# Optimization experiments

Hardware: AMD Instinct MI355X
Metric: run time of the kernel (lower is better)

## Reference

```python
import jax, jax.numpy as jnp
import numpy as np


def setup_inputs() -> dict:
    key = jax.random.key(0)
    k1, k2 = jax.random.split(key)
    query_features = jax.random.normal(k1, (8, 2048, 256), dtype=jnp.float32)   # (B, S, D)
    support_weights = jax.random.normal(k2, (20, 256), dtype=jnp.float32)       # (N, D)
    return {"query_features": query_features, "support_weights": support_weights}


def reference(query_features, support_weights):
    # Original: transpose query to (B, D, S), repeat channels n_cls times,
    # grouped conv1d with groups = n_cls*D, group_size=1, kernel_size=1, padding=0.
    # That is exactly a per-(class, channel) scale of the query features.
    B, S, D = query_features.shape
    N = support_weights.shape[0]
    q = jnp.transpose(query_features, (0, 2, 1))            # (B, D, S)
    # out[b, n, c, s] = q[b, c, s] * w[n, c]
    out = q[:, None, :, :] * support_weights[None, :, :, None]  # (B, N, D, S)
    return out.reshape(B * N, D, S)                          # (B*N, D, S)
```

## Files before the change

### kernel.cpp

```cpp
#include <hip/hip_runtime.h>


namespace {
constexpr int kB = 8;
constexpr int kS = 2048;
constexpr int kD = 256;
constexpr int kN = 20;
constexpr int TS = 512;
constexpr int TC = 16;
constexpr int NSPLIT = 2;
constexpr int NPB = kN / NSPLIT;
constexpr int PTS = TS + 4;

typedef float v4f __attribute__((ext_vector_type(4)));
}

__global__ __launch_bounds__(256)
void frw_kernel(const float* __restrict__ q, const float* __restrict__ w,
                float* __restrict__ out) {
  const int s0 = blockIdx.x * TS;
  const int c0 = blockIdx.y * TC;
  const int b  = blockIdx.z >> 1;
  const int n0 = (blockIdx.z & 1) * NPB;
  const int t  = threadIdx.x;

  __shared__ float tile[TC][PTS];
  __shared__ float ws[NPB][TC];

  for (int i = t; i < NPB * TC; i += 256) {
    const int n  = i / TC;
    const int cc = i % TC;
    ws[n][cc] = w[(n0 + n) * kD + c0 + cc];
  }

  {
    const int lane4 = t & 3;
    const int srow  = t >> 2;
    const int cvec  = lane4 * 4;
#pragma unroll
    for (int k = 0; k < 8; ++k) {
      const int ss = srow + k * 64;
      const float4 v = *reinterpret_cast<const float4*>(
          &q[((size_t)b * kS + (size_t)(s0 + ss)) * kD + (c0 + cvec)]);
      tile[cvec + 0][ss] = v.x;
      tile[cvec + 1][ss] = v.y;
      tile[cvec + 2][ss] = v.z;
      tile[cvec + 3][ss] = v.w;
    }
  }
  __syncthreads();

  const int half = t >> 7;
  const int soff = (t & 127) * 4;
  for (int nn = 0; nn < NPB; ++nn) {
    const int n = n0 + nn;
    const size_t base_bn = ((size_t)(b * kN + n)) * kD;
#pragma unroll
    for (int rg = 0; rg < TC / 2; ++rg) {
      const int r = rg * 2 + half;
      const float sc = ws[nn][r];
      const float4 v = *reinterpret_cast<const float4*>(&tile[r][soff]);
      v4f o;
      o.x = v.x * sc;
      o.y = v.y * sc;
      o.z = v.z * sc;
      o.w = v.w * sc;
      __builtin_nontemporal_store(o, reinterpret_cast<v4f*>(
          &out[(base_bn + (size_t)(c0 + r)) * kS + (size_t)(s0 + soff)]));
    }
  }
}

extern "C" void kernel_launch(void* const* d_in, const int* in_sizes, int n_in,
                              void* d_out, int out_size, void* d_ws, size_t ws_size,
                              hipStream_t stream) {
  const float* q = (const float*)d_in[0];
  const float* w = (const float*)d_in[1];
  float* out = (float*)d_out;

  dim3 grid(kS / TS, kD / TC, kB * NSPLIT);
  frw_kernel<<<grid, 256, 0, stream>>>(q, w, out);
}
```

Before: 342.8 us.

## Tile over full sequence with 8 channels and per-wave contiguous row writes

Each block now loads all 2048 sequence positions for 8 channels into shared memory, instead of 512 positions for 16 channels. Each wave then writes whole 8KB output rows for 20 (class, channel) pairs. The aim is longer contiguous store streams and fewer blocks re-reading scale weights. In exchange it uses more shared memory per block (about 66KB), launches half as many blocks, and reads the input as narrower 32-byte segments.

Measured after the change: 348.9 us. Within noise of the previous version (+1.8%).

```diff
diff --git a/kernel.cpp b/kernel.cpp
--- a/kernel.cpp
+++ b/kernel.cpp
@@ -6,11 +6,10 @@
 constexpr int kS = 2048;
 constexpr int kD = 256;
 constexpr int kN = 20;
-constexpr int TS = 512;
-constexpr int TC = 16;
+constexpr int TC = 8;
 constexpr int NSPLIT = 2;
 constexpr int NPB = kN / NSPLIT;
-constexpr int PTS = TS + 4;
+constexpr int PTS = kS + 4;
 
 typedef float v4f __attribute__((ext_vector_type(4)));
 }
@@ -18,30 +17,27 @@
 __global__ __launch_bounds__(256)
 void frw_kernel(const float* __restrict__ q, const float* __restrict__ w,
                 float* __restrict__ out) {
-  const int s0 = blockIdx.x * TS;
-  const int c0 = blockIdx.y * TC;
-  const int b  = blockIdx.z >> 1;
-  const int n0 = (blockIdx.z & 1) * NPB;
+  const int c0 = blockIdx.x * TC;
+  const int b  = blockIdx.y >> 1;
+  const int n0 = (blockIdx.y & 1) * NPB;
   const int t  = threadIdx.x;
 
   __shared__ float tile[TC][PTS];
   __shared__ float ws[NPB][TC];
 
-  for (int i = t; i < NPB * TC; i += 256) {
-    const int n  = i / TC;
-    const int cc = i % TC;
-    ws[n][cc] = w[(n0 + n) * kD + c0 + cc];
+  if (t < NPB * TC) {
+    ws[t / TC][t % TC] = w[(n0 + t / TC) * kD + c0 + (t % TC)];
   }
 
   {
-    const int lane4 = t & 3;
-    const int srow  = t >> 2;
-    const int cvec  = lane4 * 4;
+    const int lane2 = t & 1;
+    const int srow  = t >> 1;
+    const int cvec  = lane2 * 4;
 #pragma unroll
-    for (int k = 0; k < 8; ++k) {
-      const int ss = srow + k * 64;
+    for (int k = 0; k < 16; ++k) {
+      const int ss = srow + k * 128;
       const float4 v = *reinterpret_cast<const float4*>(
-          &q[((size_t)b * kS + (size_t)(s0 + ss)) * kD + (c0 + cvec)]);
+          &q[((size_t)b * kS + (size_t)ss) * kD + (c0 + cvec)]);
       tile[cvec + 0][ss] = v.x;
       tile[cvec + 1][ss] = v.y;
       tile[cvec + 2][ss] = v.z;
@@ -50,23 +46,25 @@
   }
   __syncthreads();
 
-  const int half = t >> 7;
-  const int soff = (t & 127) * 4;
-  for (int nn = 0; nn < NPB; ++nn) {
-    const int n = n0 + nn;
-    const size_t base_bn = ((size_t)(b * kN + n)) * kD;
+  const int wv   = t >> 6;
+  const int lane = t & 63;
+  for (int i = 0; i < 20; ++i) {
+    const int row = wv * 20 + i;
+    const int nn  = row >> 3;
+    const int cc  = row & 7;
+    const float sc = ws[nn][cc];
+    const size_t obase =
+        (((size_t)(b * kN + n0 + nn)) * kD + (size_t)(c0 + cc)) * (size_t)kS;
 #pragma unroll
-    for (int rg = 0; rg < TC / 2; ++rg) {
-      const int r = rg * 2 + half;
-      const float sc = ws[nn][r];
-      const float4 v = *reinterpret_cast<const float4*>(&tile[r][soff]);
+    for (int k = 0; k < 8; ++k) {
+      const int s = k * 256 + lane * 4;
+      const float4 v = *reinterpret_cast<const float4*>(&tile[cc][s]);
       v4f o;
       o.x = v.x * sc;
       o.y = v.y * sc;
       o.z = v.z * sc;
       o.w = v.w * sc;
-      __builtin_nontemporal_store(o, reinterpret_cast<v4f*>(
-          &out[(base_bn + (size_t)(c0 + r)) * kS + (size_t)(s0 + soff)]));
+      __builtin_nontemporal_store(o, reinterpret_cast<v4f*>(&out[obase + s]));
     }
   }
 }
@@ -78,6 +76,6 @@
   const float* w = (const float*)d_in[1];
   float* out = (float*)d_out;
 
-  dim3 grid(kS / TS, kD / TC, kB * NSPLIT);
+  dim3 grid(kD / TC, kB * NSPLIT, 1);
   frw_kernel<<<grid, 256, 0, stream>>>(q, w, out);
 }
```
